# Performance work log

Measured on AMD Instinct MI355X. Metric: run time of the kernel, lower is better.

## Reference

```python
import jax, jax.numpy as jnp
import numpy as np

B, T, C, H = 2, 2048, 1024, 16
HD = C // H  # head dim = 64


def setup_inputs() -> dict:
    key = jax.random.key(0)
    ks = jax.random.split(key, 5)
    s = 1.0 / np.sqrt(C)
    return {
        "x": jax.random.normal(ks[0], (B, T, C), dtype=jnp.float32),
        "W_attn": jax.random.normal(ks[1], (3 * C, C), dtype=jnp.float32) * s,
        "b_attn": jax.random.normal(ks[2], (3 * C,), dtype=jnp.float32) * 0.02,
        "W_proj": jax.random.normal(ks[3], (C, C), dtype=jnp.float32) * s,
        "b_proj": jax.random.normal(ks[4], (C,), dtype=jnp.float32) * 0.02,
    }


def reference(x, W_attn, b_attn, W_proj, b_proj):
    Bx, Tx, Cx = x.shape
    # fused QKV projection (torch Linear: x @ W.T + b)
    qkv = x @ W_attn.T + b_attn                      # [B,T,3C]
    q, k, v = jnp.split(qkv, 3, axis=-1)
    # [B,T,C] -> [B,H,T,hd]
    q = q.reshape(Bx, Tx, H, HD).transpose(0, 2, 1, 3)
    k = k.reshape(Bx, Tx, H, HD).transpose(0, 2, 1, 3)
    v = v.reshape(Bx, Tx, H, HD).transpose(0, 2, 1, 3)
    scale = 1.0 / np.sqrt(HD)
    att = jnp.einsum('bhqd,bhkd->bhqk', q, k) * scale  # [B,H,T,T]
    causal = jnp.tril(jnp.ones((Tx, Tx), dtype=bool))
    att = jnp.where(causal[None, None], att, -jnp.inf)
    att = jax.nn.softmax(att, axis=-1)
    y = jnp.einsum('bhqk,bhkd->bhqd', att, v)          # [B,H,T,hd]
    y = y.transpose(0, 2, 1, 3).reshape(Bx, Tx, Cx)
    return y @ W_proj.T + b_proj
```

## Files before the change

kernel.cpp:

```cpp
#include <hip/hip_runtime.h>

typedef unsigned short ushort_t;
typedef __bf16 bf16x8 __attribute__((ext_vector_type(8)));
typedef float f32x4 __attribute__((ext_vector_type(4)));

__device__ inline ushort_t f2bf(float f) {
  unsigned int u = __builtin_bit_cast(unsigned int, f);
  u += 0x7fff + ((u >> 16) & 1);
  return (ushort_t)(u >> 16);
}

__device__ inline unsigned pk_bf(float a, float b) {
  unsigned ua = __builtin_bit_cast(unsigned, a);
  unsigned ub = __builtin_bit_cast(unsigned, b);
  ua += 0x7fff + ((ua >> 16) & 1);
  ub += 0x7fff + ((ub >> 16) & 1);
  return __builtin_amdgcn_perm(ub, ua, 0x07060302);
}

__device__ inline void async_ld16(const ushort_t* g, const ushort_t* l) {
  __builtin_amdgcn_global_load_lds(
      (const __attribute__((address_space(1))) void*)g,
      (__attribute__((address_space(3))) void*)l, 16, 0, 0);
}

template <int IMM>
__device__ inline void waitcnt_barrier() {
  asm volatile("" ::: "memory");
  __builtin_amdgcn_s_waitcnt(IMM);
  __builtin_amdgcn_s_barrier();
  asm volatile("" ::: "memory");
}

__global__ void cvt_all(const float* __restrict__ x, const float* __restrict__ wa,
                        const float* __restrict__ wp, ushort_t* __restrict__ xb,
                        ushort_t* __restrict__ wab, ushort_t* __restrict__ wpb) {
  int i = blockIdx.x * 256 + threadIdx.x;
  const float* src;
  ushort_t* dst;
  int off;
  if (i < 1048576) { src = x; dst = xb; off = i; }
  else if (i < 1835008) { src = wa; dst = wab; off = i - 1048576; }
  else { src = wp; dst = wpb; off = i - 1835008; }
  float4 f = ((const float4*)src)[off];
  unsigned long long p = (unsigned long long)f2bf(f.x)
      | ((unsigned long long)f2bf(f.y) << 16)
      | ((unsigned long long)f2bf(f.z) << 32)
      | ((unsigned long long)f2bf(f.w) << 48);
  ((unsigned long long*)dst)[off] = p;
}

template <int BM, int BN, int IM, int JN, int MODE, int TPB>
__global__ __launch_bounds__(TPB) void gemm_bt(
    const ushort_t* __restrict__ A, const ushort_t* __restrict__ B,
    const float* __restrict__ bias, float* __restrict__ Cf,
    ushort_t* __restrict__ Cb, ushort_t* __restrict__ vtb,
    int M, int N, int K, int ldc, float qscale) {
  constexpr int NWN = BN / (JN * 16);
  constexpr int NL = (BM + BN) * 32 / (TPB * 8);
  constexpr int WIMM = 0x0F70 | NL;
  __shared__ __align__(16) ushort_t As[3][BM * 32];
  __shared__ __align__(16) ushort_t Bs[3][BN * 32];
  const int tid = threadIdx.x;
  const int wave = tid >> 6, lane = tid & 63;
  const int quad = lane >> 4, l16 = lane & 15;
  const int wr = wave / NWN, wc = wave % NWN;
  const int wm = wr * IM * 16, wn = wc * JN * 16;
  const int m0 = blockIdx.y * BM, n0 = blockIdx.x * BN;
  const ushort_t* Ag = A + (size_t)m0 * K;
  const ushort_t* Bg = B + (size_t)n0 * K;
  const int slot = (quad ^ ((l16 >> 1) & 3)) * 8;
  f32x4 acc[IM][JN] = {};

  auto stage = [&](int kt, int bsel) {
    int k0 = kt * 32;
#pragma unroll
    for (int p = 0; p < BM * 4 / TPB; ++p) {
      int ci = p * TPB + tid;
      int row = ci >> 2, ch = (ci & 3) ^ ((ci >> 3) & 3);
      async_ld16(Ag + (size_t)row * K + k0 + ch * 8, As[bsel] + (p * TPB + wave * 64) * 8);
    }
#pragma unroll
    for (int p = 0; p < BN * 4 / TPB; ++p) {
      int ci = p * TPB + tid;
      int row = ci >> 2, ch = (ci & 3) ^ ((ci >> 3) & 3);
      async_ld16(Bg + (size_t)row * K + k0 + ch * 8, Bs[bsel] + (p * TPB + wave * 64) * 8);
    }
  };

  const int KT = K / 32;
  stage(0, 0);
  stage(1, 1);
  for (int kt = 0; kt < KT; ++kt) {
    waitcnt_barrier<WIMM>();
    if (kt + 2 < KT) stage(kt + 2, (kt + 2) % 3);
    const ushort_t* Ac = As[kt % 3];
    const ushort_t* Bc = Bs[kt % 3];
    bf16x8 af[IM], bfr[JN];
#pragma unroll
    for (int i = 0; i < IM; ++i)
      af[i] = *(const bf16x8*)(Ac + (wm + i * 16 + l16) * 32 + slot);
#pragma unroll
    for (int j = 0; j < JN; ++j)
      bfr[j] = *(const bf16x8*)(Bc + (wn + j * 16 + l16) * 32 + slot);
#pragma unroll
    for (int i = 0; i < IM; ++i)
#pragma unroll
      for (int j = 0; j < JN; ++j)
        acc[i][j] = __builtin_amdgcn_mfma_f32_16x16x32_bf16(af[i], bfr[j], acc[i][j], 0, 0, 0);
  }

  if (MODE == 1 && n0 >= 2048) {
#pragma unroll
    for (int j = 0; j < JN; ++j) {
      int col = n0 + wn + j * 16 + l16;
      int cv = col - 2048;
      float bv = bias[col];
      size_t rowbase = ((size_t)(cv >> 6)) * 64 + (cv & 63);
#pragma unroll
      for (int i = 0; i < IM; ++i) {
        int rowb = m0 + wm + i * 16 + quad * 4;
        int bb = rowb >> 11, t = rowb & 2047;
        uint2 pp;
        pp.x = pk_bf(acc[i][j][0] + bv, acc[i][j][1] + bv);
        pp.y = pk_bf(acc[i][j][2] + bv, acc[i][j][3] + bv);
        *(uint2*)(vtb + (((size_t)bb * 1024 + rowbase) * 2048 + t)) = pp;
      }
    }
    return;
  }
#pragma unroll
  for (int j = 0; j < JN; ++j) {
    int col = n0 + wn + j * 16 + l16;
    float bv = bias[col];
    float sc = (MODE == 1 && col < 1024) ? qscale : 1.0f;
#pragma unroll
    for (int i = 0; i < IM; ++i)
#pragma unroll
      for (int r = 0; r < 4; ++r) {
        int row = m0 + wm + i * 16 + quad * 4 + r;
        float v = (acc[i][j][r] + bv) * sc;
        if (MODE == 1)
          Cb[(size_t)row * ldc + col] = f2bf(v);
        else
          Cf[(size_t)row * ldc + col] = v;
      }
  }
}

__global__ __launch_bounds__(256, 3) void flash6(
    const ushort_t* __restrict__ qk, const ushort_t* __restrict__ vt,
    ushort_t* __restrict__ y) {
  __shared__ __align__(16) ushort_t Kb[2][4096];
  __shared__ __align__(16) ushort_t Vb[2][4096];
  __shared__ __align__(16) ushort_t Ps[4][32 * 72];
  const int tid = threadIdx.x, wave = tid >> 6, lane = tid & 63;
  const int quad = lane >> 4, l16 = lane & 15;
  const int r7 = l16 & 7;
  const int xx = blockIdx.x, bh = blockIdx.y;
  const int Q = (bh < 16) ? (15 - xx) : xx;
  const int b = bh >> 4, h = bh & 15;
  const int bT = b * 2048;
  const int qw = Q * 128 + wave * 32;
  ushort_t* Pw = Ps[wave];

  bf16x8 qf[2][2];
#pragma unroll
  for (int f = 0; f < 2; ++f) {
    const ushort_t* qrow = qk + (size_t)(bT + qw + f * 16 + l16) * 2048 + h * 64 + quad * 8;
    qf[f][0] = *(const bf16x8*)(qrow);
    qf[f][1] = *(const bf16x8*)(qrow + 32);
  }

  auto stage = [&](int kt, int bsel) {
    int k0 = kt * 64;
#pragma unroll
    for (int i = 0; i < 2; ++i) {
      int ci = i * 256 + tid;
      int row = ci >> 3, ch = (ci & 7) ^ (row & 7);
      async_ld16(qk + (size_t)(bT + k0 + row) * 2048 + 1024 + h * 64 + ch * 8,
                 Kb[bsel] + (i * 256 + wave * 64) * 8);
      async_ld16(vt + (size_t)(bh * 64 + row) * 2048 + k0 + ch * 8,
                 Vb[bsel] + (i * 256 + wave * 64) * 8);
    }
  };

  f32x4 o[4][2] = {};
  float lac[2] = {0.f, 0.f};
  const int KT = 2 * Q + 2;

  stage(0, 0);
  for (int kt = 0; kt < KT; ++kt) {
    const int cur = kt & 1;
    waitcnt_barrier<0x0F70>();
    if (kt + 1 < KT) stage(kt + 1, cur ^ 1);
    const ushort_t* Kc = Kb[cur];
    const ushort_t* Vc = Vb[cur];
    bf16x8 kf[4][2];
#pragma unroll
    for (int j = 0; j < 4; ++j)
#pragma unroll
      for (int ks = 0; ks < 2; ++ks)
        kf[j][ks] = *(const bf16x8*)(Kc + (j * 16 + l16) * 64 + (((ks * 4 + quad) ^ r7) * 8));
    f32x4 s[4][2] = {};
#pragma unroll
    for (int ks = 0; ks < 2; ++ks)
#pragma unroll
      for (int j = 0; j < 4; ++j) {
        s[j][0] = __builtin_amdgcn_mfma_f32_16x16x32_bf16(kf[j][ks], qf[0][ks], s[j][0], 0, 0, 0);
        s[j][1] = __builtin_amdgcn_mfma_f32_16x16x32_bf16(kf[j][ks], qf[1][ks], s[j][1], 0, 0, 0);
      }
    if (kt >= KT - 2) {
#pragma unroll
      for (int f = 0; f < 2; ++f) {
        int qloc = qw + f * 16 + l16;
#pragma unroll
        for (int j = 0; j < 4; ++j)
#pragma unroll
          for (int r = 0; r < 4; ++r)
            if (kt * 64 + j * 16 + quad * 4 + r > qloc) s[j][f][r] = -1e30f;
      }
    }
#pragma unroll
    for (int f = 0; f < 2; ++f)
#pragma unroll
      for (int j = 0; j < 4; ++j) {
#pragma unroll
        for (int r = 0; r < 4; ++r) {
          float pv = exp2f(s[j][f][r]);
          s[j][f][r] = pv;
          lac[f] += pv;
        }
        uint2 pp;
        pp.x = pk_bf(s[j][f][0], s[j][f][1]);
        pp.y = pk_bf(s[j][f][2], s[j][f][3]);
        *(uint2*)(Pw + (f * 16 + l16) * 72 + j * 16 + quad * 4) = pp;
      }
    __builtin_amdgcn_s_waitcnt(0xc07f);
    bf16x8 pf[2][2];
#pragma unroll
    for (int ks = 0; ks < 2; ++ks)
#pragma unroll
      for (int f = 0; f < 2; ++f)
        pf[ks][f] = *(const bf16x8*)(Pw + (f * 16 + l16) * 72 + ks * 32 + quad * 8);
#pragma unroll
    for (int ks = 0; ks < 2; ++ks)
#pragma unroll
      for (int j = 0; j < 4; ++j) {
        bf16x8 vf = *(const bf16x8*)(Vc + (j * 16 + l16) * 64 + (((ks * 4 + quad) ^ r7) * 8));
        o[j][0] = __builtin_amdgcn_mfma_f32_16x16x32_bf16(vf, pf[ks][0], o[j][0], 0, 0, 0);
        o[j][1] = __builtin_amdgcn_mfma_f32_16x16x32_bf16(vf, pf[ks][1], o[j][1], 0, 0, 0);
      }
  }

#pragma unroll
  for (int f = 0; f < 2; ++f) {
    float l = lac[f];
    l += __shfl_xor(l, 16, 64);
    l += __shfl_xor(l, 32, 64);
    float inv = 1.f / l;
    size_t row = (size_t)(bT + qw + f * 16 + l16);
#pragma unroll
    for (int j = 0; j < 4; ++j) {
      uint2 pp;
      pp.x = pk_bf(o[j][f][0] * inv, o[j][f][1] * inv);
      pp.y = pk_bf(o[j][f][2] * inv, o[j][f][3] * inv);
      *(uint2*)(y + row * 1024 + h * 64 + j * 16 + quad * 4) = pp;
    }
  }
}

extern "C" void kernel_launch(void* const* d_in, const int* in_sizes, int n_in,
                              void* d_out, int out_size, void* d_ws, size_t ws_size,
                              hipStream_t stream) {
  const float* x  = (const float*)d_in[0];
  const float* Wa = (const float*)d_in[1];
  const float* ba = (const float*)d_in[2];
  const float* Wp = (const float*)d_in[3];
  const float* bp = (const float*)d_in[4];
  float* out = (float*)d_out;
  char* ws = (char*)d_ws;
  ushort_t* xb  = (ushort_t*)(ws);
  ushort_t* Wab = (ushort_t*)(ws + 8388608);
  ushort_t* Wpb = (ushort_t*)(ws + 14680064);
  ushort_t* qkb = (ushort_t*)(ws + 16777216);
  ushort_t* yb  = (ushort_t*)(ws + 33554432);
  ushort_t* vtb = (ushort_t*)(ws + 41943040);

  cvt_all<<<8192, 256, 0, stream>>>(x, Wa, Wp, xb, Wab, Wpb);
  gemm_bt<128, 128, 4, 2, 1, 512><<<dim3(24, 32), 512, 0, stream>>>(
      xb, Wab, ba, nullptr, qkb, vtb, 4096, 3072, 1024, 2048, 0.18033688011112042f);
  flash6<<<dim3(16, 32), 256, 0, stream>>>(qkb, vtb, yb);
  gemm_bt<64, 64, 2, 2, 0, 256><<<dim3(16, 64), 256, 0, stream>>>(
      yb, Wpb, bp, out, nullptr, nullptr, 4096, 1024, 1024, 1024, 1.0f);
}
```

Before: 195.0 us.

## Keep P in registers via permuted K layout, triple-buffer K/V, use hardware bf16 pack

Changes the K-row mapping so each lane's score accumulators line up with the B-operand layout of the PV MFMA. P can then be packed straight from registers, removing the LDS round-trip for P along with its waitcnt. The K/V staging goes from double to triple buffering with a two-tile prefetch distance, and launch bounds drop to 2 blocks per CU. bf16 packing now uses the v_cvt_pk_bf16_f32 instruction. This costs more LDS per block and possibly lower occupancy, and it depends on the K swizzle and mask index remap being correct.

```diff
diff --git a/kernel.cpp b/kernel.cpp
--- a/kernel.cpp
+++ b/kernel.cpp
@@ -3,6 +3,7 @@
 typedef unsigned short ushort_t;
 typedef __bf16 bf16x8 __attribute__((ext_vector_type(8)));
 typedef float f32x4 __attribute__((ext_vector_type(4)));
+typedef unsigned u32x4 __attribute__((ext_vector_type(4)));
 
 __device__ inline ushort_t f2bf(float f) {
   unsigned int u = __builtin_bit_cast(unsigned int, f);
@@ -11,11 +12,9 @@
 }
 
 __device__ inline unsigned pk_bf(float a, float b) {
-  unsigned ua = __builtin_bit_cast(unsigned, a);
-  unsigned ub = __builtin_bit_cast(unsigned, b);
-  ua += 0x7fff + ((ua >> 16) & 1);
-  ub += 0x7fff + ((ub >> 16) & 1);
-  return __builtin_amdgcn_perm(ub, ua, 0x07060302);
+  unsigned r;
+  asm("v_cvt_pk_bf16_f32 %0, %1, %2" : "=v"(r) : "v"(a), "v"(b));
+  return r;
 }
 
 __device__ inline void async_ld16(const ushort_t* g, const ushort_t* l) {
@@ -148,21 +147,21 @@
   }
 }
 
-__global__ __launch_bounds__(256, 3) void flash6(
+__global__ __launch_bounds__(256, 2) void flash7(
     const ushort_t* __restrict__ qk, const ushort_t* __restrict__ vt,
     ushort_t* __restrict__ y) {
-  __shared__ __align__(16) ushort_t Kb[2][4096];
-  __shared__ __align__(16) ushort_t Vb[2][4096];
-  __shared__ __align__(16) ushort_t Ps[4][32 * 72];
+  __shared__ __align__(16) ushort_t Kb[3][4096];
+  __shared__ __align__(16) ushort_t Vb[3][4096];
   const int tid = threadIdx.x, wave = tid >> 6, lane = tid & 63;
   const int quad = lane >> 4, l16 = lane & 15;
   const int r7 = l16 & 7;
+  const int fK = (l16 & 3) | (((l16 >> 2) & 1) << 2);
+  const int kbase = (16 * (l16 >> 2) + (l16 & 3)) * 64;
   const int xx = blockIdx.x, bh = blockIdx.y;
   const int Q = (bh < 16) ? (15 - xx) : xx;
   const int b = bh >> 4, h = bh & 15;
   const int bT = b * 2048;
   const int qw = Q * 128 + wave * 32;
-  ushort_t* Pw = Ps[wave];
 
   bf16x8 qf[2][2];
 #pragma unroll
@@ -177,10 +176,12 @@
 #pragma unroll
     for (int i = 0; i < 2; ++i) {
       int ci = i * 256 + tid;
-      int row = ci >> 3, ch = (ci & 7) ^ (row & 7);
-      async_ld16(qk + (size_t)(bT + k0 + row) * 2048 + 1024 + h * 64 + ch * 8,
+      int row = ci >> 3;
+      int chk = (ci & 7) ^ ((row & 3) | (((row >> 4) & 1) << 2));
+      int chv = (ci & 7) ^ (row & 7);
+      async_ld16(qk + (size_t)(bT + k0 + row) * 2048 + 1024 + h * 64 + chk * 8,
                  Kb[bsel] + (i * 256 + wave * 64) * 8);
-      async_ld16(vt + (size_t)(bh * 64 + row) * 2048 + k0 + ch * 8,
+      async_ld16(vt + (size_t)(bh * 64 + row) * 2048 + k0 + chv * 8,
                  Vb[bsel] + (i * 256 + wave * 64) * 8);
     }
   };
@@ -190,10 +191,12 @@
   const int KT = 2 * Q + 2;
 
   stage(0, 0);
+  stage(1, 1);
   for (int kt = 0; kt < KT; ++kt) {
-    const int cur = kt & 1;
-    waitcnt_barrier<0x0F70>();
-    if (kt + 1 < KT) stage(kt + 1, cur ^ 1);
+    const int cur = kt % 3;
+    if (kt + 1 < KT) waitcnt_barrier<0x0F74>();
+    else             waitcnt_barrier<0x0F70>();
+    if (kt + 2 < KT) stage(kt + 2, (kt + 2) % 3);
     const ushort_t* Kc = Kb[cur];
     const ushort_t* Vc = Vb[cur];
     bf16x8 kf[4][2];
@@ -201,7 +204,7 @@
     for (int j = 0; j < 4; ++j)
 #pragma unroll
       for (int ks = 0; ks < 2; ++ks)
-        kf[j][ks] = *(const bf16x8*)(Kc + (j * 16 + l16) * 64 + (((ks * 4 + quad) ^ r7) * 8));
+        kf[j][ks] = *(const bf16x8*)(Kc + kbase + j * 256 + (((ks * 4 + quad) ^ fK) * 8));
     f32x4 s[4][2] = {};
 #pragma unroll
     for (int ks = 0; ks < 2; ++ks)
@@ -218,36 +221,36 @@
         for (int j = 0; j < 4; ++j)
 #pragma unroll
           for (int r = 0; r < 4; ++r)
-            if (kt * 64 + j * 16 + quad * 4 + r > qloc) s[j][f][r] = -1e30f;
+            if (kt * 64 + quad * 16 + j * 4 + r > qloc) s[j][f][r] = -1e30f;
       }
     }
 #pragma unroll
     for (int f = 0; f < 2; ++f)
 #pragma unroll
-      for (int j = 0; j < 4; ++j) {
+      for (int j = 0; j < 4; ++j)
 #pragma unroll
         for (int r = 0; r < 4; ++r) {
           float pv = exp2f(s[j][f][r]);
           s[j][f][r] = pv;
           lac[f] += pv;
         }
-        uint2 pp;
-        pp.x = pk_bf(s[j][f][0], s[j][f][1]);
-        pp.y = pk_bf(s[j][f][2], s[j][f][3]);
-        *(uint2*)(Pw + (f * 16 + l16) * 72 + j * 16 + quad * 4) = pp;
-      }
-    __builtin_amdgcn_s_waitcnt(0xc07f);
     bf16x8 pf[2][2];
 #pragma unroll
     for (int ks = 0; ks < 2; ++ks)
 #pragma unroll
-      for (int f = 0; f < 2; ++f)
-        pf[ks][f] = *(const bf16x8*)(Pw + (f * 16 + l16) * 72 + ks * 32 + quad * 8);
+      for (int f = 0; f < 2; ++f) {
+        u32x4 w;
+        w[0] = pk_bf(s[2 * ks][f][0], s[2 * ks][f][1]);
+        w[1] = pk_bf(s[2 * ks][f][2], s[2 * ks][f][3]);
+        w[2] = pk_bf(s[2 * ks + 1][f][0], s[2 * ks + 1][f][1]);
+        w[3] = pk_bf(s[2 * ks + 1][f][2], s[2 * ks + 1][f][3]);
+        pf[ks][f] = __builtin_bit_cast(bf16x8, w);
+      }
 #pragma unroll
     for (int ks = 0; ks < 2; ++ks)
 #pragma unroll
       for (int j = 0; j < 4; ++j) {
-        bf16x8 vf = *(const bf16x8*)(Vc + (j * 16 + l16) * 64 + (((ks * 4 + quad) ^ r7) * 8));
+        bf16x8 vf = *(const bf16x8*)(Vc + (j * 16 + l16) * 64 + (((ks + 2 * quad) ^ r7) * 8));
         o[j][0] = __builtin_amdgcn_mfma_f32_16x16x32_bf16(vf, pf[ks][0], o[j][0], 0, 0, 0);
         o[j][1] = __builtin_amdgcn_mfma_f32_16x16x32_bf16(vf, pf[ks][1], o[j][1], 0, 0, 0);
       }
@@ -290,7 +293,7 @@
   cvt_all<<<8192, 256, 0, stream>>>(x, Wa, Wp, xb, Wab, Wpb);
   gemm_bt<128, 128, 4, 2, 1, 512><<<dim3(24, 32), 512, 0, stream>>>(
       xb, Wab, ba, nullptr, qkb, vtb, 4096, 3072, 1024, 2048, 0.18033688011112042f);
-  flash6<<<dim3(16, 32), 256, 0, stream>>>(qkb, vtb, yb);
+  flash7<<<dim3(16, 32), 256, 0, stream>>>(qkb, vtb, yb);
   gemm_bt<64, 64, 2, 2, 0, 256><<<dim3(16, 64), 256, 0, stream>>>(
       yb, Wpb, bp, out, nullptr, nullptr, 4096, 1024, 1024, 1024, 1.0f);
 }
```

After: 188.8 us. 3.2% less time.
